# Optimization experiments

Measured on AMD Instinct MI355X. Metric: run time of the kernel, lower is better.

Reference implementation:

```python
import jax, jax.numpy as jnp
import numpy as np

ALPHABET = 8
DIM = 128
SEQ_LEN = 8192
POWER_ITERS = 200


def setup_inputs() -> dict:
    key = jax.random.key(0)
    k1, k2, k3 = jax.random.split(key, 3)
    return {
        "Kraus_op_re": jax.random.uniform(k1, (ALPHABET, DIM, DIM), dtype=jnp.float32),
        "Kraus_op_im": jax.random.uniform(k2, (ALPHABET, DIM, DIM), dtype=jnp.float32),
        "sequence": jax.random.randint(k3, (SEQ_LEN,), 0, ALPHABET),
    }


def _leading_eig(K):
    # K: [A, d, d] complex. Power iteration on the transfer map and its adjoint.
    d = K.shape[-1]
    Kc = K.conj()

    def body_r(rhor, _):
        # rhov = sum_x K_x @ rhor @ K_x^H
        rhov = jnp.einsum("aij,jk,alk->il", K, rhor, Kc)
        mu = jnp.trace(rhov).real
        return rhov / mu.astype(rhov.dtype), None

    rhor, _ = jax.lax.scan(body_r, jnp.eye(d, dtype=K.dtype) / d, None, length=POWER_ITERS)

    def body_l(carry, _):
        rhol, _ = carry
        # rhov = sum_x K_x^H @ rhol @ K_x
        rhov = jnp.einsum("aji,jk,akl->il", Kc, rhol, K)
        mu = jnp.trace(rhov).real
        return (rhov / mu.astype(rhov.dtype), mu), None

    (rhol, mu), _ = jax.lax.scan(
        body_l, (jnp.eye(d, dtype=K.dtype), jnp.asarray(1.0, jnp.float32)), None, length=POWER_ITERS
    )
    return rhor, rhol, mu


def reference(Kraus_op_re, Kraus_op_im, sequence):
    K = Kraus_op_re.astype(jnp.complex64) + 1j * Kraus_op_im.astype(jnp.complex64)
    rhor, rhol, lam = _leading_eig(K)
    # normalize so that trace(rho @ rhol) == 1
    rho0 = rhor / jnp.trace(rhor @ rhol).real.astype(rhor.dtype)
    Kn = K / jnp.sqrt(lam).astype(K.dtype)  # Kraus ops rescaled by sqrt(leading eigenvalue)
    L = sequence.shape[0]

    def step(carry, inp):
        rho, logp = carry
        i, x = inp
        Kx = Kn[x]
        rho = Kx @ rho @ Kx.conj().T
        px = jnp.where(i == L - 1, jnp.trace(rho @ rhol).real, jnp.trace(rho).real)
        logp = logp - jnp.log2(px)
        rho = rho / px.astype(rho.dtype)
        return (rho, logp), None

    (_, log_p), _ = jax.lax.scan(
        step, (rho0, jnp.asarray(0.0, jnp.float32)), (jnp.arange(L), sequence)
    )
    return log_p[None]  # matches torch.tensor([0.0]) accumulator shape (1,)
```

## Files before the change

kernel.cpp:

```cpp
#include <hip/hip_runtime.h>

typedef unsigned int u32;
typedef unsigned short u16;
typedef __attribute__((ext_vector_type(4))) float f32x4;
typedef __attribute__((ext_vector_type(8))) short s16x8;
typedef __attribute__((ext_vector_type(4))) u32 u32x4;

#define DIMN 128
#define MATN (DIMN*DIMN)
#define NA 8
#define LSEQ 8192
#define NTOK (LSEQ/2)
#define PITERS 4
#define S1SH 5
#define S2SH 6
#define CHSH 7
#define P2SH 8
#define GCH 256
#define GLG 16

struct WS {
  u16 *Kb, *P2b, *rho, *nodes0, *nodes1, *rootR, *rootI;
  int *tok, *E0, *E1, *Eroot;
  float *trbuf;
  float *out;
};

__device__ __forceinline__ u16 f2bf(float x){
  u32 u = __float_as_uint(x);
  u32 r = (u + 0x7FFFu + ((u >> 16) & 1u)) >> 16;
  return (u16)r;
}
__device__ __forceinline__ float bf2f(u16 u){ return __uint_as_float(((u32)u) << 16); }
__device__ __forceinline__ u32 cvtpk(float lo, float hi){
  u32 r; asm("v_cvt_pk_bf16_f32 %0, %1, %2" : "=v"(r) : "v"(lo), "v"(hi)); return r;
}
__device__ __forceinline__ s16x8 negi(s16x8 v){
  return __builtin_bit_cast(s16x8, __builtin_bit_cast(u32x4, v) ^ 0x80008000u);
}
__device__ __forceinline__ int swz16(int maj, int b){
  return maj*256 + (((((b >> 4) + maj*5) & 15) << 4) | (b & 15));
}
template<int CA, int CB>
__device__ __forceinline__ void cmfma(s16x8 a_r, s16x8 a_i, s16x8 b_r, s16x8 b_i,
                                      f32x4& qr, f32x4& qi){
  s16x8 t1 = (CA ^ CB) ? a_i : negi(a_i);
  s16x8 t2 = CB ? negi(a_r) : a_r;
  s16x8 t3 = CA ? negi(a_i) : a_i;
  qr = __builtin_amdgcn_mfma_f32_16x16x32_bf16(a_r, b_r, qr, 0,0,0);
  qr = __builtin_amdgcn_mfma_f32_16x16x32_bf16(t1,  b_i, qr, 0,0,0);
  qi = __builtin_amdgcn_mfma_f32_16x16x32_bf16(t2,  b_i, qi, 0,0,0);
  qi = __builtin_amdgcn_mfma_f32_16x16x32_bf16(t3,  b_r, qi, 0,0,0);
}

__global__ __launch_bounds__(256) void k_kbinit(const float* Kre, const float* Kim,
                                                const int* seq, WS w){
  __shared__ u16 Lr[32][36], Li[32][36];
  int blk = blockIdx.x, x = blk >> 4, tile = blk & 15;
  int row0 = (tile>>2)*32, col0 = (tile&3)*32;
  int t = threadIdx.x;
  { int r = t>>3, cch = t&7;
    size_t off = (size_t)x*MATN + (size_t)(row0+r)*128 + col0 + cch*4;
    float4 vr = *(const float4*)(Kre + off);
    float4 vi = *(const float4*)(Kim + off);
    Lr[r][cch*4+0] = f2bf(vr.x); Lr[r][cch*4+1] = f2bf(vr.y);
    Lr[r][cch*4+2] = f2bf(vr.z); Lr[r][cch*4+3] = f2bf(vr.w);
    Li[r][cch*4+0] = f2bf(vi.x); Li[r][cch*4+1] = f2bf(vi.y);
    Li[r][cch*4+2] = f2bf(vi.z); Li[r][cch*4+3] = f2bf(vi.w);
  }
  __syncthreads();
  u16* b = w.Kb + (size_t)x*4*MATN;
  { int r = t>>3, cch = t&7;
    *(uint2*)&b[(row0+r)*128 + col0 + cch*4]        = *(uint2*)&Lr[r][cch*4];
    *(uint2*)&b[MATN + (row0+r)*128 + col0 + cch*4] = *(uint2*)&Li[r][cch*4];
  }
  { int c = t>>3, rch = t&7;
    ushort4 vr, vi;
    vr.x = Lr[rch*4+0][c]; vr.y = Lr[rch*4+1][c];
    vr.z = Lr[rch*4+2][c]; vr.w = Lr[rch*4+3][c];
    vi.x = Li[rch*4+0][c]; vi.y = Li[rch*4+1][c];
    vi.z = Li[rch*4+2][c]; vi.w = Li[rch*4+3][c];
    *(ushort4*)&b[2*MATN + (col0+c)*128 + row0 + rch*4] = vr;
    *(ushort4*)&b[3*MATN + (col0+c)*128 + row0 + rch*4] = vi;
  }
  int gid = blockIdx.x*256 + t, gsz = gridDim.x*256;
  for (int i = gid; i < NTOK; i += gsz)
    w.tok[i] = seq[2*i+1]*NA + seq[2*i];
  for (int i = gid; i < 4*MATN; i += gsz){
    int plane = (i >> 14) & 1, rem = i & (MATN-1);
    u16 v = (plane == 0 && (rem >> 7) == (rem & 127)) ? f2bf(1.f) : (u16)0;
    w.rho[i] = v;
  }
  if (gid < 32) w.trbuf[gid] = 0.f;
}

__device__ __forceinline__ void ccompute(const u16* Ar, const u16* Ai,
    const char* Pr, const char* Pi, f32x4 (&qr)[2][4], f32x4 (&qi)[2][4], int t){
  int wv = t>>6, lane = t&63, l15 = lane&15, hi = lane>>4;
  int wr = (wv>>1)*32, wc = (wv&1)*64;
  #pragma unroll
  for (int m=0;m<2;m++)
    #pragma unroll
    for (int n=0;n<4;n++){ qr[m][n] = (f32x4){0,0,0,0}; qi[m][n] = (f32x4){0,0,0,0}; }
  #pragma unroll
  for (int kk = 0; kk < 4; kk++){
    int kb = kk*32 + hi*8;
    s16x8 a_r[2], a_i[2];
    #pragma unroll
    for (int m=0;m<2;m++){
      int r = wr + m*16 + l15;
      a_r[m] = *(const s16x8*)(Ar + r*128 + kb);
      a_i[m] = *(const s16x8*)(Ai + r*128 + kb);
    }
    #pragma unroll
    for (int n=0;n<4;n++){
      int c = wc + n*16 + l15;
      int o = swz16(c, kb*2);
      s16x8 b_r = *(const s16x8*)(Pr + o);
      s16x8 b_i = *(const s16x8*)(Pi + o);
      #pragma unroll
      for (int m=0;m<2;m++)
        cmfma<0,0>(a_r[m], a_i[m], b_r, b_i, qr[m][n], qi[m][n]);
    }
  }
}
__device__ __forceinline__ void pwrite16(char* Pr, char* Pi,
    f32x4 (&qr)[2][4], f32x4 (&qi)[2][4], float sc, int t){
  int wv = t>>6, lane = t&63, l15 = lane&15, hi = lane>>4;
  int wr = (wv>>1)*32, wc = (wv&1)*64;
  #pragma unroll
  for (int m=0;m<2;m++)
    #pragma unroll
    for (int n=0;n<4;n++){
      int c = wc + n*16 + l15, r0 = wr + m*16 + hi*4;
      uint2 pr, pi;
      pr.x = cvtpk(qr[m][n][0]*sc, qr[m][n][1]*sc);
      pr.y = cvtpk(qr[m][n][2]*sc, qr[m][n][3]*sc);
      pi.x = cvtpk(qi[m][n][0]*sc, qi[m][n][1]*sc);
      pi.y = cvtpk(qi[m][n][2]*sc, qi[m][n][3]*sc);
      int o = swz16(c, r0*2);
      *(uint2*)(Pr + o) = pr;
      *(uint2*)(Pi + o) = pi;
    }
}
__device__ __forceinline__ int renorm_to(char* Pr, char* Pi, float* red,
    f32x4 (&qr)[2][4], f32x4 (&qi)[2][4], int t){
  int wv = t>>6, lane = t&63;
  float lm = 0.f;
  #pragma unroll
  for (int m=0;m<2;m++)
    #pragma unroll
    for (int n=0;n<4;n++)
      #pragma unroll
      for (int j=0;j<4;j++)
        lm = fmaxf(lm, fmaxf(fabsf(qr[m][n][j]), fabsf(qi[m][n][j])));
  #pragma unroll
  for (int o = 32; o > 0; o >>= 1) lm = fmaxf(lm, __shfl_xor(lm, o, 64));
  if (lane == 0) red[wv] = lm;
  __syncthreads();
  float mx = 0.f;
  #pragma unroll
  for (int i = 0; i < 8; i++) mx = fmaxf(mx, red[i]);
  int e = 0; if (mx > 0.f) frexpf(mx, &e);
  pwrite16(Pr, Pi, qr, qi, ldexpf(1.f, -e), t);
  return e;
}
__device__ __forceinline__ void stage_cols16(const u16* gr, const u16* gi,
                                             char* Pr, char* Pi, int t){
  #pragma unroll
  for (int i = 0; i < 4; i++){
    int chunk = t + i*512;
    int c = chunk >> 4, rr = chunk & 15;
    int o = swz16(c, rr*16);
    *(uint4*)(Pr + o) = *(const uint4*)(gr + c*128 + rr*8);
    *(uint4*)(Pi + o) = *(const uint4*)(gi + c*128 + rr*8);
  }
}
__device__ __forceinline__ void write_node16(u16* dr, u16* di,
    const char* Pr, const char* Pi, bool rowLayout, int t){
  if (!rowLayout){
    #pragma unroll
    for (int i = 0; i < 4; i++){
      int chunk = t + i*512;
      int c = chunk >> 4, rr = chunk & 15;
      int o = swz16(c, rr*16);
      *(uint4*)(dr + c*128 + rr*8) = *(const uint4*)(Pr + o);
      *(uint4*)(di + c*128 + rr*8) = *(const uint4*)(Pi + o);
    }
  } else {
    for (int idx = t; idx < MATN; idx += 512){
      int r = idx >> 7, c = idx & 127;
      int o = swz16(c, r*2);
      dr[idx] = *(const u16*)(Pr + o);
      di[idx] = *(const u16*)(Pi + o);
    }
  }
}

__global__ __launch_bounds__(512) void k_p2m(WS w){
  __shared__ __align__(16) char P0r[32768];
  __shared__ __align__(16) char P0i[32768];
  __shared__ __align__(16) char P1r[32768];
  __shared__ __align__(16) char P1i[32768];
  int blk = blockIdx.x, a = blk >> 3, b = blk & 7;
  int t = threadIdx.x;
  const u16* Bb = w.Kb + (size_t)(b*4 + 2)*MATN;
  stage_cols16(Bb, Bb + MATN, P0r, P0i, t);
  __syncthreads();
  const u16* Ab = w.Kb + (size_t)(a*4)*MATN;
  f32x4 qr[2][4], qi[2][4];
  ccompute(Ab, Ab + MATN, P0r, P0i, qr, qi, t);
  pwrite16(P1r, P1i, qr, qi, 1.f/(1<<P2SH), t);
  __syncthreads();
  u16* base = w.P2b + (size_t)blk*4*MATN;
  write_node16(base + 2*MATN, base + 3*MATN, P1r, P1i, false, t);
  write_node16(base, base + MATN, P1r, P1i, true, t);
}

__global__ __launch_bounds__(512,2) void k_chain(WS w){
  __shared__ __align__(16) char P0r[32768];
  __shared__ __align__(16) char P0i[32768];
  __shared__ __align__(16) char P1r[32768];
  __shared__ __align__(16) char P1i[32768];
  __shared__ float red[8];
  int p = blockIdx.x, t = threadIdx.x;
  char *PrC = P0r, *PiC = P0i, *PrN = P1r, *PiN = P1i;
  int tok0 = w.tok[p*GLG];
  const u16* b0 = w.P2b + (size_t)tok0*4*MATN;
  stage_cols16(b0 + 2*MATN, b0 + 3*MATN, PrC, PiC, t);
  f32x4 qr[2][4], qi[2][4];
  int eLast = 0;
  __syncthreads();
  #pragma unroll 1
  for (int s = 1; s < GLG; s++){
    const u16* tb = w.P2b + (size_t)w.tok[p*GLG + s]*4*MATN;
    ccompute(tb, tb + MATN, PrC, PiC, qr, qi, t);
    if (s < GLG-1) pwrite16(PrN, PiN, qr, qi, 1.f/(1<<CHSH), t);
    else eLast = renorm_to(PrN, PiN, red, qr, qi, t);
    __syncthreads();
    { char* x = PrC; PrC = PrN; PrN = x; x = PiC; PiC = PiN; PiN = x; }
  }
  u16* slot = w.nodes0 + (size_t)p*2*MATN;
  write_node16(slot, slot + MATN, PrC, PiC, (p & 3) != 0, t);
  if (t == 0) w.E0[p] = P2SH*GLG + CHSH*(GLG-2) + eLast;
}

__global__ __launch_bounds__(512,2) void k_level(WS w, int srcIs0, int isRoot){
  __shared__ __align__(16) char P0r[32768];
  __shared__ __align__(16) char P0i[32768];
  __shared__ __align__(16) char P1r[32768];
  __shared__ __align__(16) char P1i[32768];
  __shared__ float red[8];
  int p = blockIdx.x, t = threadIdx.x;
  char *PrC = P0r, *PiC = P0i, *PrN = P1r, *PiN = P1i;
  const u16* src = srcIs0 ? w.nodes0 : w.nodes1;
  u16* dst       = srcIs0 ? w.nodes1 : w.nodes0;
  const int* Es  = srcIs0 ? w.E0 : w.E1;
  int* Ed        = srcIs0 ? w.E1 : w.E0;
  const u16* B = src + (size_t)(4*p)*2*MATN;
  stage_cols16(B, B + MATN, PrC, PiC, t);
  int E = Es[4*p] + Es[4*p+1] + Es[4*p+2] + Es[4*p+3];
  f32x4 qr[2][4], qi[2][4];
  __syncthreads();
  #pragma unroll 1
  for (int j = 1; j < 4; j++){
    const u16* A = src + (size_t)(4*p + j)*2*MATN;
    ccompute(A, A + MATN, PrC, PiC, qr, qi, t);
    E += renorm_to(PrN, PiN, red, qr, qi, t);
    __syncthreads();
    { char* x = PrC; PrC = PrN; PrN = x; x = PiC; PiC = PiN; PiN = x; }
  }
  u16* slot = dst + (size_t)p*2*MATN;
  write_node16(slot, slot + MATN, PrC, PiC, ((p & 3) != 0) || isRoot, t);
  if (t == 0) Ed[p] = E;
}

__global__ __launch_bounds__(512,1) void k_pow(WS w, int par){
  __shared__ __align__(16) char Rr[32768];
  __shared__ __align__(16) char Ri[32768];
  __shared__ __align__(16) char Yr[32768];
  __shared__ __align__(16) char Yi[32768];
  int b = blockIdx.x, side = b >> 3, rb = b & 7;
  int t = threadIdx.x, wv = t>>6, lane = t&63, l15 = lane&15, hi = lane>>4;
  const u16* rhoS = w.rho + (size_t)((par*2 + side)*2)*MATN;
  stage_cols16(rhoS, rhoS + MATN, Rr, Ri, t);
  __syncthreads();
  { int x = wv;
    const u16* Ab = w.Kb + (size_t)(x*4 + (side ? 2 : 0))*MATN;
    const u16* Ar = Ab; const u16* Ai = Ab + MATN;
    f32x4 q1r[8], q1i[8];
    #pragma unroll
    for (int n=0;n<8;n++){ q1r[n] = (f32x4){0,0,0,0}; q1i[n] = (f32x4){0,0,0,0}; }
    #pragma unroll
    for (int kk = 0; kk < 4; kk++){
      int kb = kk*32 + hi*8;
      int r = rb*16 + l15;
      s16x8 a_r = *(const s16x8*)(Ar + r*128 + kb);
      s16x8 a_i = *(const s16x8*)(Ai + r*128 + kb);
      #pragma unroll
      for (int n=0;n<8;n++){
        int c = n*16 + l15;
        int o = swz16(c, kb*2);
        s16x8 b_r = *(const s16x8*)(Rr + o);
        s16x8 b_i = *(const s16x8*)(Ri + o);
        if (side == 0) cmfma<0,0>(a_r, a_i, b_r, b_i, q1r[n], q1i[n]);
        else           cmfma<1,0>(a_r, a_i, b_r, b_i, q1r[n], q1i[n]);
      }
    }
    const float sc = 1.f/(1<<S1SH);
    #pragma unroll
    for (int n=0;n<8;n++)
      #pragma unroll
      for (int q=0;q<4;q++){
        int lr = hi*4 + q, c = n*16 + l15;
        *(u16*)(Yr + x*4096 + swz16(lr, c*2)) = f2bf(q1r[n][q]*sc);
        *(u16*)(Yi + x*4096 + swz16(lr, c*2)) = f2bf(q1i[n][q]*sc);
      }
  }
  __syncthreads();
  { int c0 = wv*16, c = c0 + l15;
    f32x4 q2r = {0,0,0,0}, q2i = {0,0,0,0};
    #pragma unroll 2
    for (int x = 0; x < 8; x++){
      const u16* Bb = w.Kb + (size_t)(x*4 + (side ? 2 : 0))*MATN;
      const u16* Br = Bb; const u16* Bi = Bb + MATN;
      #pragma unroll
      for (int kk = 0; kk < 4; kk++){
        int kb = kk*32 + hi*8;
        s16x8 a_r = *(const s16x8*)(Yr + x*4096 + swz16(l15, kb*2));
        s16x8 a_i = *(const s16x8*)(Yi + x*4096 + swz16(l15, kb*2));
        s16x8 b_r = *(const s16x8*)(Br + c*128 + kb);
        s16x8 b_i = *(const s16x8*)(Bi + c*128 + kb);
        if (side == 0) cmfma<0,1>(a_r, a_i, b_r, b_i, q2r, q2i);
        else           cmfma<0,0>(a_r, a_i, b_r, b_i, q2r, q2i);
      }
    }
    const float sc = 1.f/(1<<S2SH);
    u16* Dr = w.rho + (size_t)(((par^1)*2 + side)*2)*MATN;
    u16* Di = Dr + MATN;
    int r0g = rb*16 + hi*4;
    uint2 pr, pi;
    pr.x = cvtpk(q2r[0]*sc, q2r[1]*sc); pr.y = cvtpk(q2r[2]*sc, q2r[3]*sc);
    pi.x = cvtpk(q2i[0]*sc, q2i[1]*sc); pi.y = cvtpk(q2i[2]*sc, q2i[3]*sc);
    *(uint2*)(Dr + c*128 + r0g) = pr;
    *(uint2*)(Di + c*128 + r0g) = pi;
    if (side == 1 && wv == rb){
      float tr = 0.f;
      #pragma unroll
      for (int q=0;q<4;q++) if (hi*4 + q == l15) tr += q2r[q]*sc;
      #pragma unroll
      for (int o = 32; o > 0; o >>= 1) tr += __shfl_xor(tr, o, 64);
      if (lane == 0) w.trbuf[par*16 + 8 + rb] = tr;
    }
  }
}

__global__ __launch_bounds__(512) void k_epi(WS w){
  __shared__ __align__(16) char T1r[32768];
  __shared__ __align__(16) char T1i[32768];
  int t = threadIdx.x, wv = t>>6, lane = t&63, l15 = lane&15, hi = lane>>4;
  int wr = (wv>>2)*64, wc = (wv&3)*32;
  f32x4 qr[4][2], qi[4][2];
  const u16* Ar = w.rho;
  const u16* Ai = Ar + MATN;
  #pragma unroll
  for (int m=0;m<4;m++)
    #pragma unroll
    for (int n=0;n<2;n++){ qr[m][n] = (f32x4){0,0,0,0}; qi[m][n] = (f32x4){0,0,0,0}; }
  #pragma unroll
  for (int kk = 0; kk < 4; kk++){
    int kb = kk*32 + hi*8;
    #pragma unroll
    for (int m=0;m<4;m++){
      int r = wr + m*16 + l15;
      s16x8 a_r = *(const s16x8*)(Ar + r*128 + kb);
      s16x8 a_i = *(const s16x8*)(Ai + r*128 + kb);
      #pragma unroll
      for (int n=0;n<2;n++){
        int c = wc + n*16 + l15;
        s16x8 b_r = *(const s16x8*)(w.rootR + c*128 + kb);
        s16x8 b_i = *(const s16x8*)(w.rootI + c*128 + kb);
        cmfma<0,0>(a_r, a_i, b_r, b_i, qr[m][n], qi[m][n]);
      }
    }
  }
  {
    const float sc = 1.f/(1<<CHSH);
    #pragma unroll
    for (int m=0;m<4;m++)
      #pragma unroll
      for (int n=0;n<2;n++){
        int c = wc + n*16 + l15, r0 = wr + m*16 + hi*4;
        uint2 pr, pi;
        pr.x = cvtpk(qr[m][n][0]*sc, qr[m][n][1]*sc);
        pr.y = cvtpk(qr[m][n][2]*sc, qr[m][n][3]*sc);
        pi.x = cvtpk(qi[m][n][0]*sc, qi[m][n][1]*sc);
        pi.y = cvtpk(qi[m][n][2]*sc, qi[m][n][3]*sc);
        int o = swz16(c, r0*2);
        *(uint2*)(T1r + o) = pr;
        *(uint2*)(T1i + o) = pi;
      }
  }
  __syncthreads();
  #pragma unroll
  for (int m=0;m<4;m++)
    #pragma unroll
    for (int n=0;n<2;n++){ qr[m][n] = (f32x4){0,0,0,0}; qi[m][n] = (f32x4){0,0,0,0}; }
  #pragma unroll
  for (int kk = 0; kk < 4; kk++){
    int kb = kk*32 + hi*8;
    #pragma unroll
    for (int m=0;m<4;m++){
      int r = wr + m*16 + l15;
      int o = swz16(r, kb*2);
      s16x8 a_r = *(const s16x8*)(T1r + o);
      s16x8 a_i = *(const s16x8*)(T1i + o);
      #pragma unroll
      for (int n=0;n<2;n++){
        int c = wc + n*16 + l15;
        s16x8 b_r = *(const s16x8*)(w.rootR + c*128 + kb);
        s16x8 b_i = *(const s16x8*)(w.rootI + c*128 + kb);
        cmfma<0,1>(a_r, a_i, b_r, b_i, qr[m][n], qi[m][n]);
      }
    }
  }
  __syncthreads();
  double* red = (double*)T1r;
  const u16* rlr = w.rho + (size_t)2*MATN;
  const u16* rli = rlr + MATN;
  double a1 = 0.0;
  #pragma unroll
  for (int m=0;m<4;m++)
    #pragma unroll
    for (int n=0;n<2;n++){
      int c = wc + n*16 + l15, r0 = wr + m*16 + hi*4;
      #pragma unroll
      for (int q=0;q<4;q++){
        int r = r0 + q;
        float lr = bf2f(rlr[r*128 + c]), li = bf2f(rli[r*128 + c]);
        a1 += (double)qr[m][n][q]*lr - (double)qi[m][n][q]*li;
      }
    }
  red[t] = a1; __syncthreads();
  for (int o = 256; o > 0; o >>= 1){ if (t < o) red[t] += red[t+o]; __syncthreads(); }
  double that = red[0]; __syncthreads();
  const u16* rrr = w.rho;
  const u16* rri = rrr + MATN;
  double a2 = 0.0;
  for (int idx = t; idx < MATN; idx += 512){
    int c = idx >> 7, r = idx & 127;
    float ar_ = bf2f(rrr[idx]), ai_ = bf2f(rri[idx]);
    float lr  = bf2f(rlr[r*128 + c]), li = bf2f(rli[r*128 + c]);
    a2 += (double)ar_*lr - (double)ai_*li;
  }
  red[t] = a2; __syncthreads();
  for (int o = 256; o > 0; o >>= 1){ if (t < o) red[t] += red[t+o]; __syncthreads(); }
  double trrl = red[0];
  if (t == 0){
    double T0 = 0.0, T1s = 0.0;
    for (int s = 0; s < 8; s++){ T0 += w.trbuf[8+s]; T1s += w.trbuf[16+8+s]; }
    double lam = ldexp(T1s / T0, S1SH + S2SH);
    double logp = (double)LSEQ * log2(lam) - 2.0*(double)w.Eroot[0] - (double)CHSH
                  - log2(fmax(that, 1e-300)) + log2(fmax(trrl, 1e-300));
    w.out[0] = (float)logp;
  }
}

static inline size_t aln256(size_t x){ return (x + 255) & ~(size_t)255; }

extern "C" void kernel_launch(void* const* d_in, const int* in_sizes, int n_in,
                              void* d_out, int out_size, void* d_ws, size_t ws_size,
                              hipStream_t stream){
  const float* Kre = (const float*)d_in[0];
  const float* Kim = (const float*)d_in[1];
  const int*   seq = (const int*)d_in[2];

  WS w{};
  char* p = (char*)d_ws;
  auto take = [&](size_t bytes)->char*{ char* r = p; p += aln256(bytes); return r; };
  w.Kb    = (u16*)take((size_t)NA*4*MATN*2);
  w.P2b   = (u16*)take((size_t)64*4*MATN*2);
  w.rho   = (u16*)take((size_t)8*MATN*2);
  w.nodes0= (u16*)take((size_t)GCH*2*MATN*2);
  w.nodes1= (u16*)take((size_t)(GCH/4)*2*MATN*2);
  w.tok   = (int*)take(NTOK*4);
  w.E0    = (int*)take(GCH*4);
  w.E1    = (int*)take(GCH*4);
  w.trbuf = (float*)take(32*4);
  w.out = (float*)d_out;
  w.rootR = w.nodes0; w.rootI = w.nodes0 + MATN;
  w.Eroot = w.E0;

  hipLaunchKernelGGL(k_kbinit, dim3(NA*16), dim3(256), 0, stream, Kre, Kim, seq, w);
  hipLaunchKernelGGL(k_p2m, dim3(64), dim3(512), 0, stream, w);
  hipLaunchKernelGGL(k_chain, dim3(GCH), dim3(512), 0, stream, w);
  hipLaunchKernelGGL(k_level, dim3(64), dim3(512), 0, stream, w, 1, 0);
  hipLaunchKernelGGL(k_level, dim3(16), dim3(512), 0, stream, w, 0, 0);
  hipLaunchKernelGGL(k_level, dim3(4),  dim3(512), 0, stream, w, 1, 0);
  hipLaunchKernelGGL(k_level, dim3(1),  dim3(512), 0, stream, w, 0, 1);
  for (int k = 0; k < PITERS; k++)
    hipLaunchKernelGGL(k_pow, dim3(16), dim3(512), 0, stream, w, k & 1);
  hipLaunchKernelGGL(k_epi, dim3(1), dim3(512), 0, stream, w);
}
```

Baseline: 310.0 us.

## Prefetch next A-operand fragments into registers during chain and level products

Splits the complex matrix product so the A-matrix fragments are loaded from global memory into registers once per step, and issues the load for the next step's operand right after the current MFMA work. Global latency can then overlap with the LDS write and barrier. The full __syncthreads is replaced by an LDS-only waitcnt plus s_barrier, so in-flight global loads are not drained at the barrier. Launch bounds drop to one block per CU to make room for the extra registers (16 more s16x8 per thread), which reduces occupancy.

```diff
diff --git a/kernel.cpp b/kernel.cpp
--- a/kernel.cpp
+++ b/kernel.cpp
@@ -94,24 +94,29 @@
   if (gid < 32) w.trbuf[gid] = 0.f;
 }
 
-__device__ __forceinline__ void ccompute(const u16* Ar, const u16* Ai,
-    const char* Pr, const char* Pi, f32x4 (&qr)[2][4], f32x4 (&qi)[2][4], int t){
-  int wv = t>>6, lane = t&63, l15 = lane&15, hi = lane>>4;
-  int wr = (wv>>1)*32, wc = (wv&1)*64;
-  #pragma unroll
-  for (int m=0;m<2;m++)
-    #pragma unroll
-    for (int n=0;n<4;n++){ qr[m][n] = (f32x4){0,0,0,0}; qi[m][n] = (f32x4){0,0,0,0}; }
+__device__ __forceinline__ void loadA(const u16* Ar, const u16* Ai,
+    int wr, int l15, int hi, s16x8 (&fr)[4][2], s16x8 (&fi)[4][2]){
   #pragma unroll
   for (int kk = 0; kk < 4; kk++){
     int kb = kk*32 + hi*8;
-    s16x8 a_r[2], a_i[2];
-    #pragma unroll
-    for (int m=0;m<2;m++){
+    #pragma unroll
+    for (int m = 0; m < 2; m++){
       int r = wr + m*16 + l15;
-      a_r[m] = *(const s16x8*)(Ar + r*128 + kb);
-      a_i[m] = *(const s16x8*)(Ai + r*128 + kb);
-    }
+      fr[kk][m] = *(const s16x8*)(Ar + r*128 + kb);
+      fi[kk][m] = *(const s16x8*)(Ai + r*128 + kb);
+    }
+  }
+}
+__device__ __forceinline__ void ccomputeR(const s16x8 (&fr)[4][2], const s16x8 (&fi)[4][2],
+    const char* Pr, const char* Pi, f32x4 (&qr)[2][4], f32x4 (&qi)[2][4],
+    int wc, int l15, int hi){
+  #pragma unroll
+  for (int m=0;m<2;m++)
+    #pragma unroll
+    for (int n=0;n<4;n++){ qr[m][n] = (f32x4){0,0,0,0}; qi[m][n] = (f32x4){0,0,0,0}; }
+  #pragma unroll
+  for (int kk = 0; kk < 4; kk++){
+    int kb = kk*32 + hi*8;
     #pragma unroll
     for (int n=0;n<4;n++){
       int c = wc + n*16 + l15;
@@ -120,7 +125,7 @@
       s16x8 b_i = *(const s16x8*)(Pi + o);
       #pragma unroll
       for (int m=0;m<2;m++)
-        cmfma<0,0>(a_r[m], a_i[m], b_r, b_i, qr[m][n], qi[m][n]);
+        cmfma<0,0>(fr[kk][m], fi[kk][m], b_r, b_i, qr[m][n], qi[m][n]);
     }
   }
 }
@@ -203,13 +208,16 @@
   __shared__ __align__(16) char P1r[32768];
   __shared__ __align__(16) char P1i[32768];
   int blk = blockIdx.x, a = blk >> 3, b = blk & 7;
-  int t = threadIdx.x;
+  int t = threadIdx.x, wv = t>>6, lane = t&63, l15 = lane&15, hi = lane>>4;
+  int wr = (wv>>1)*32, wc = (wv&1)*64;
   const u16* Bb = w.Kb + (size_t)(b*4 + 2)*MATN;
   stage_cols16(Bb, Bb + MATN, P0r, P0i, t);
-  __syncthreads();
+  s16x8 Afr[4][2], Afi[4][2];
   const u16* Ab = w.Kb + (size_t)(a*4)*MATN;
+  loadA(Ab, Ab + MATN, wr, l15, hi, Afr, Afi);
+  __syncthreads();
   f32x4 qr[2][4], qi[2][4];
-  ccompute(Ab, Ab + MATN, P0r, P0i, qr, qi, t);
+  ccomputeR(Afr, Afi, P0r, P0i, qr, qi, wc, l15, hi);
   pwrite16(P1r, P1i, qr, qi, 1.f/(1<<P2SH), t);
   __syncthreads();
   u16* base = w.P2b + (size_t)blk*4*MATN;
@@ -217,27 +225,36 @@
   write_node16(base, base + MATN, P1r, P1i, true, t);
 }
 
-__global__ __launch_bounds__(512,2) void k_chain(WS w){
+__global__ __launch_bounds__(512,1) void k_chain(WS w){
   __shared__ __align__(16) char P0r[32768];
   __shared__ __align__(16) char P0i[32768];
   __shared__ __align__(16) char P1r[32768];
   __shared__ __align__(16) char P1i[32768];
   __shared__ float red[8];
   int p = blockIdx.x, t = threadIdx.x;
+  int wv = t>>6, lane = t&63, l15 = lane&15, hi = lane>>4;
+  int wr = (wv>>1)*32, wc = (wv&1)*64;
   char *PrC = P0r, *PiC = P0i, *PrN = P1r, *PiN = P1i;
   int tok0 = w.tok[p*GLG];
   const u16* b0 = w.P2b + (size_t)tok0*4*MATN;
   stage_cols16(b0 + 2*MATN, b0 + 3*MATN, PrC, PiC, t);
+  s16x8 Afr[4][2], Afi[4][2];
+  { const u16* tb = w.P2b + (size_t)w.tok[p*GLG + 1]*4*MATN;
+    loadA(tb, tb + MATN, wr, l15, hi, Afr, Afi); }
   f32x4 qr[2][4], qi[2][4];
   int eLast = 0;
   __syncthreads();
   #pragma unroll 1
   for (int s = 1; s < GLG; s++){
-    const u16* tb = w.P2b + (size_t)w.tok[p*GLG + s]*4*MATN;
-    ccompute(tb, tb + MATN, PrC, PiC, qr, qi, t);
+    ccomputeR(Afr, Afi, PrC, PiC, qr, qi, wc, l15, hi);
+    if (s + 1 < GLG){
+      const u16* tb = w.P2b + (size_t)w.tok[p*GLG + s + 1]*4*MATN;
+      loadA(tb, tb + MATN, wr, l15, hi, Afr, Afi);
+    }
     if (s < GLG-1) pwrite16(PrN, PiN, qr, qi, 1.f/(1<<CHSH), t);
     else eLast = renorm_to(PrN, PiN, red, qr, qi, t);
-    __syncthreads();
+    asm volatile("s_waitcnt lgkmcnt(0)" ::: "memory");
+    __builtin_amdgcn_s_barrier();
     { char* x = PrC; PrC = PrN; PrN = x; x = PiC; PiC = PiN; PiN = x; }
   }
   u16* slot = w.nodes0 + (size_t)p*2*MATN;
@@ -245,13 +262,15 @@
   if (t == 0) w.E0[p] = P2SH*GLG + CHSH*(GLG-2) + eLast;
 }
 
-__global__ __launch_bounds__(512,2) void k_level(WS w, int srcIs0, int isRoot){
+__global__ __launch_bounds__(512,1) void k_level(WS w, int srcIs0, int isRoot){
   __shared__ __align__(16) char P0r[32768];
   __shared__ __align__(16) char P0i[32768];
   __shared__ __align__(16) char P1r[32768];
   __shared__ __align__(16) char P1i[32768];
   __shared__ float red[8];
   int p = blockIdx.x, t = threadIdx.x;
+  int wv = t>>6, lane = t&63, l15 = lane&15, hi = lane>>4;
+  int wr = (wv>>1)*32, wc = (wv&1)*64;
   char *PrC = P0r, *PiC = P0i, *PrN = P1r, *PiN = P1i;
   const u16* src = srcIs0 ? w.nodes0 : w.nodes1;
   u16* dst       = srcIs0 ? w.nodes1 : w.nodes0;
@@ -259,15 +278,22 @@
   int* Ed        = srcIs0 ? w.E1 : w.E0;
   const u16* B = src + (size_t)(4*p)*2*MATN;
   stage_cols16(B, B + MATN, PrC, PiC, t);
+  s16x8 Afr[4][2], Afi[4][2];
+  { const u16* A = src + (size_t)(4*p+1)*2*MATN;
+    loadA(A, A + MATN, wr, l15, hi, Afr, Afi); }
   int E = Es[4*p] + Es[4*p+1] + Es[4*p+2] + Es[4*p+3];
   f32x4 qr[2][4], qi[2][4];
   __syncthreads();
   #pragma unroll 1
   for (int j = 1; j < 4; j++){
-    const u16* A = src + (size_t)(4*p + j)*2*MATN;
-    ccompute(A, A + MATN, PrC, PiC, qr, qi, t);
+    ccomputeR(Afr, Afi, PrC, PiC, qr, qi, wc, l15, hi);
+    if (j < 3){
+      const u16* A = src + (size_t)(4*p + j + 1)*2*MATN;
+      loadA(A, A + MATN, wr, l15, hi, Afr, Afi);
+    }
     E += renorm_to(PrN, PiN, red, qr, qi, t);
-    __syncthreads();
+    asm volatile("s_waitcnt lgkmcnt(0)" ::: "memory");
+    __builtin_amdgcn_s_barrier();
     { char* x = PrC; PrC = PrN; PrN = x; x = PiC; PiC = PiN; PiN = x; }
   }
   u16* slot = dst + (size_t)p*2*MATN;
```

New measurement: 305.9 us. About the same (-1.3%).
